# Performance work log

Hardware: AMD Instinct MI355X
Metric: run time of the kernel (lower is better)

The kernel has to match this reference:

```python
import jax, jax.numpy as jnp
import numpy as np

# Tokenizer hyperparams (match init_kwargs)
NUM_VARS = 8
EMBED = 64
WIN = 16
STEP = 4
SWIDTH = 1.0  # sample_width
PWIDTH = 1.0  # patch_width
BATCH = 32
SAMPLES = 4096


def setup_inputs() -> dict:
    key = jax.random.key(0)
    k1, k2, k3, k4, k5 = jax.random.split(key, 5)
    return {
        "x": jax.random.normal(k1, (BATCH, NUM_VARS, SAMPLES), dtype=jnp.float32),
        "W1": jax.random.normal(k2, (NUM_VARS, EMBED), dtype=jnp.float32),   # sample-level LSH hyperplanes
        "b1": jax.random.normal(k3, (EMBED,), dtype=jnp.float32),
        "W2": jax.random.normal(k4, (WIN * EMBED, EMBED), dtype=jnp.float32),  # patch-level LSH hyperplanes
        "b2": jax.random.normal(k5, (EMBED,), dtype=jnp.float32),
    }


def reference(x, W1, b1, W2, b2):
    B, V, S = x.shape
    # encode(): per-timestep sample-level LSH hash, fully vectorized over S.
    # torch loop does sample_level(x[:,:,ix]) for each ix -> one batched einsum here.
    # e: [B, EMBED, S]
    e = jnp.floor((jnp.einsum('bvs,vd->bds', x, W1) + b1[None, :, None]) / SWIDTH)

    # quantize(): sliding windows over the time axis.
    starts = jnp.arange(0, S - WIN, STEP)                 # [T] window start positions
    idx = starts[:, None] + jnp.arange(WIN)[None, :]
    wins = e[:, :, idx]
    T = starts.shape[0]
    flat = wins.transpose(0, 2, 1, 3).reshape(B, T, EMBED * WIN)
    # patch-level LSH hash per window
    tokens = jnp.floor((jnp.einsum('btf,fe->bte', flat, W2) + b2) / PWIDTH)  # [B, T, EMBED]
    return tokens
```

## Files before the change

### kernel.cpp

```cpp
#include <hip/hip_runtime.h>
#include <cstdint>
#include <cstddef>

#define B_ 32
#define V_ 8
#define S_ 4096
#define E_ 64
#define T_ 1020
#define TT 32
#define SLP 200

typedef __bf16 bf16_t;
typedef bf16_t bf16x8 __attribute__((ext_vector_type(8)));
typedef float f32x4 __attribute__((ext_vector_type(4)));
typedef unsigned long long u64;
typedef u64 u64x2 __attribute__((ext_vector_type(2)));

__global__ __launch_bounds__(256) void prep_kernel(const float* __restrict__ W2,
                                                   bf16_t* __restrict__ w2sw) {
  const int q = blockIdx.x * 256 + threadIdx.x;
  const int l = q & 63, nt = (q >> 6) & 3, kk = q >> 8;
  const int fb = kk * 32 + (l >> 4) * 8;
  const int n = nt * 16 + (l & 15);
  bf16x8 v;
#pragma unroll
  for (int j = 0; j < 8; ++j) v[j] = (bf16_t)W2[(fb + j) * E_ + n];
  *reinterpret_cast<bf16x8*>(w2sw + (size_t)q * 8) = v;
}

__global__ __launch_bounds__(256, 4) void fused_kernel(const float* __restrict__ x,
                                                       const float* __restrict__ W1,
                                                       const float* __restrict__ b1,
                                                       const bf16_t* __restrict__ w2sw,
                                                       const float* __restrict__ b2,
                                                       float* __restrict__ out) {
  __shared__ bf16_t et[E_ * SLP];
  const int tid = threadIdx.x;
  const int b = blockIdx.y;
  const int t0 = blockIdx.x * TT;
  const int lane = tid & 63;
  const int wvu = __builtin_amdgcn_readfirstlane(tid >> 6);
  const int l15 = lane & 15;
  const int g = lane >> 4;
  const int s0 = 4 * t0;

  int sc[3];
#pragma unroll
  for (int k = 0; k < 3; ++k) {
    int s = s0 + lane + 64 * k;
    sc[k] = (s > S_ - 1) ? (S_ - 1) : s;
  }
  float xv[V_][3];
#pragma unroll
  for (int v = 0; v < V_; ++v) {
    const float* xb = x + ((size_t)(b * V_ + v) << 12);
#pragma unroll
    for (int k = 0; k < 3; ++k) xv[v][k] = xb[sc[k]];
  }
  const bf16_t* bptr = w2sw + (((size_t)wvu * 64 + lane) << 3);
  bf16x8 bpre[16];
#pragma unroll
  for (int kk = 0; kk < 16; ++kk) {
    bpre[kk] = *reinterpret_cast<const bf16x8*>(bptr + ((size_t)kk << 11));
    u64x2 t = __builtin_bit_cast(u64x2, bpre[kk]);
    asm volatile("" : "+v"(t[0]), "+v"(t[1]));
    bpre[kk] = __builtin_bit_cast(bf16x8, t);
  }

  const int dbase = wvu * 16;
  const float* w1w = W1 + dbase;
  const float* b1w = b1 + dbase;
#pragma unroll
  for (int dd = 0; dd < 16; ++dd) {
    const float bb = b1w[dd];
    float a0 = bb, a1 = bb, a2 = bb;
#pragma unroll
    for (int v = 0; v < V_; ++v) {
      const float w = w1w[v * E_ + dd];
      a0 += xv[v][0] * w;
      a1 += xv[v][1] * w;
      a2 += xv[v][2] * w;
    }
    const int row = (dbase + dd) * SLP;
    et[row + lane]      = (bf16_t)floorf(a0);
    et[row + lane + 64] = (bf16_t)floorf(a1);
    if (lane < 12) et[row + lane + 128] = (bf16_t)floorf(a2);
  }
  __syncthreads();

  const char* etb = reinterpret_cast<const char*>(et);
  const uint32_t aoff = 400u * (g >> 1) + 8u * l15 + 16u * (g & 1);
  const float bv = b2[wvu * 16 + l15];
  f32x4 acc0 = {bv, bv, bv, bv};
  f32x4 acc1 = {bv, bv, bv, bv};
#pragma unroll
  for (int kk = 0; kk < 16; ++kk) {
    const char* pa = etb + aoff + 800 * kk;
    union { u64 q[2]; bf16x8 v; } A0, A1;
    A0.q[0] = *reinterpret_cast<const u64*>(pa);
    A0.q[1] = *reinterpret_cast<const u64*>(pa + 8);
    A1.q[0] = *reinterpret_cast<const u64*>(pa + 128);
    A1.q[1] = *reinterpret_cast<const u64*>(pa + 136);
    acc0 = __builtin_amdgcn_mfma_f32_16x16x32_bf16(A0.v, bpre[kk], acc0, 0, 0, 0);
    acc1 = __builtin_amdgcn_mfma_f32_16x16x32_bf16(A1.v, bpre[kk], acc1, 0, 0, 0);
  }
#pragma unroll 8
  for (int kk = 16; kk < 32; ++kk) {
    const char* pa = etb + aoff + 800 * kk;
    union { u64 q[2]; bf16x8 v; } A0, A1;
    A0.q[0] = *reinterpret_cast<const u64*>(pa);
    A0.q[1] = *reinterpret_cast<const u64*>(pa + 8);
    A1.q[0] = *reinterpret_cast<const u64*>(pa + 128);
    A1.q[1] = *reinterpret_cast<const u64*>(pa + 136);
    const bf16x8 Bf = *reinterpret_cast<const bf16x8*>(bptr + ((size_t)kk << 11));
    acc0 = __builtin_amdgcn_mfma_f32_16x16x32_bf16(A0.v, Bf, acc0, 0, 0, 0);
    acc1 = __builtin_amdgcn_mfma_f32_16x16x32_bf16(A1.v, Bf, acc1, 0, 0, 0);
  }
#pragma unroll
  for (int r = 0; r < 4; ++r) {
    const int t1 = t0 + g * 4 + r;
    if (t1 < T_)
      __builtin_nontemporal_store(floorf(acc0[r]),
                                  &out[((size_t)(b * T_ + t1)) * E_ + wvu * 16 + l15]);
    const int t2 = t0 + 16 + g * 4 + r;
    if (t2 < T_)
      __builtin_nontemporal_store(floorf(acc1[r]),
                                  &out[((size_t)(b * T_ + t2)) * E_ + wvu * 16 + l15]);
  }
}

extern "C" void kernel_launch(void* const* d_in, const int* in_sizes, int n_in,
                              void* d_out, int out_size, void* d_ws, size_t ws_size,
                              hipStream_t stream) {
  const float* x  = (const float*)d_in[0];
  const float* W1 = (const float*)d_in[1];
  const float* b1 = (const float*)d_in[2];
  const float* W2 = (const float*)d_in[3];
  const float* b2 = (const float*)d_in[4];
  float* out = (float*)d_out;

  bf16_t* w2sw = (bf16_t*)d_ws;

  hipLaunchKernelGGL(prep_kernel, dim3(32), dim3(256), 0, stream, W2, w2sw);
  hipLaunchKernelGGL(fused_kernel, dim3((T_ + TT - 1) / TT, B_), dim3(256), 0, stream,
                     x, W1, b1, w2sw, b2, out);
}
```

Measured before the change: 23.17 us.

## Vectorize x loads, pack bf16 LDS stores, drop B-fragment register prefetch

Each lane now loads two adjacent x samples as a float2, plus a small tail handled by six lanes, instead of three strided scalar loads. It writes two bf16 values per 32-bit LDS store instead of single 16-bit stores. The 16-entry register prefetch of W2 fragments, which was overlapped with the sample-level stage, is removed; all 32 k-steps now load B from global memory inside the MFMA loop. This cuts register pressure and LDS store count, at the cost of losing the overlap of B loads with the first stage's compute.

```diff
diff --git a/kernel.cpp b/kernel.cpp
--- a/kernel.cpp
+++ b/kernel.cpp
@@ -14,7 +14,6 @@
 typedef bf16_t bf16x8 __attribute__((ext_vector_type(8)));
 typedef float f32x4 __attribute__((ext_vector_type(4)));
 typedef unsigned long long u64;
-typedef u64 u64x2 __attribute__((ext_vector_type(2)));
 
 __global__ __launch_bounds__(256) void prep_kernel(const float* __restrict__ W2,
                                                    bf16_t* __restrict__ w2sw) {
@@ -26,6 +25,13 @@
 #pragma unroll
   for (int j = 0; j < 8; ++j) v[j] = (bf16_t)W2[(fb + j) * E_ + n];
   *reinterpret_cast<bf16x8*>(w2sw + (size_t)q * 8) = v;
+}
+
+__device__ __forceinline__ uint32_t pack2bf(float a, float b) {
+  union { bf16_t h[2]; uint32_t u; } p;
+  p.h[0] = (bf16_t)a;
+  p.h[1] = (bf16_t)b;
+  return p.u;
 }
 
 __global__ __launch_bounds__(256, 4) void fused_kernel(const float* __restrict__ x,
@@ -44,68 +50,51 @@
   const int g = lane >> 4;
   const int s0 = 4 * t0;
 
-  int sc[3];
-#pragma unroll
-  for (int k = 0; k < 3; ++k) {
-    int s = s0 + lane + 64 * k;
-    sc[k] = (s > S_ - 1) ? (S_ - 1) : s;
-  }
-  float xv[V_][3];
+  float2 xm[V_];
+  float xt0[V_], xt1[V_];
+  const bool htail = lane < 6;
+  int sa = s0 + 128 + 2 * lane, sb = sa + 1;
+  if (sa > S_ - 1) sa = S_ - 1;
+  if (sb > S_ - 1) sb = S_ - 1;
 #pragma unroll
   for (int v = 0; v < V_; ++v) {
     const float* xb = x + ((size_t)(b * V_ + v) << 12);
-#pragma unroll
-    for (int k = 0; k < 3; ++k) xv[v][k] = xb[sc[k]];
-  }
-  const bf16_t* bptr = w2sw + (((size_t)wvu * 64 + lane) << 3);
-  bf16x8 bpre[16];
-#pragma unroll
-  for (int kk = 0; kk < 16; ++kk) {
-    bpre[kk] = *reinterpret_cast<const bf16x8*>(bptr + ((size_t)kk << 11));
-    u64x2 t = __builtin_bit_cast(u64x2, bpre[kk]);
-    asm volatile("" : "+v"(t[0]), "+v"(t[1]));
-    bpre[kk] = __builtin_bit_cast(bf16x8, t);
+    xm[v] = *reinterpret_cast<const float2*>(xb + s0 + 2 * lane);
+    xt0[v] = htail ? xb[sa] : 0.0f;
+    xt1[v] = htail ? xb[sb] : 0.0f;
   }
 
+  char* etc = reinterpret_cast<char*>(et);
   const int dbase = wvu * 16;
-  const float* w1w = W1 + dbase;
-  const float* b1w = b1 + dbase;
 #pragma unroll
   for (int dd = 0; dd < 16; ++dd) {
-    const float bb = b1w[dd];
-    float a0 = bb, a1 = bb, a2 = bb;
+    const int d = dbase + dd;
+    const float bb = b1[d];
+    float a0 = bb, a1 = bb, c0 = bb, c1 = bb;
 #pragma unroll
     for (int v = 0; v < V_; ++v) {
-      const float w = w1w[v * E_ + dd];
-      a0 += xv[v][0] * w;
-      a1 += xv[v][1] * w;
-      a2 += xv[v][2] * w;
+      const float w = W1[v * E_ + d];
+      a0 += xm[v].x * w;
+      a1 += xm[v].y * w;
+      c0 += xt0[v] * w;
+      c1 += xt1[v] * w;
     }
-    const int row = (dbase + dd) * SLP;
-    et[row + lane]      = (bf16_t)floorf(a0);
-    et[row + lane + 64] = (bf16_t)floorf(a1);
-    if (lane < 12) et[row + lane + 128] = (bf16_t)floorf(a2);
+    *reinterpret_cast<uint32_t*>(etc + d * 400 + 4 * lane) =
+        pack2bf(floorf(a0), floorf(a1));
+    if (htail)
+      *reinterpret_cast<uint32_t*>(etc + d * 400 + 256 + 4 * lane) =
+          pack2bf(floorf(c0), floorf(c1));
   }
   __syncthreads();
 
   const char* etb = reinterpret_cast<const char*>(et);
   const uint32_t aoff = 400u * (g >> 1) + 8u * l15 + 16u * (g & 1);
+  const bf16_t* bptr = w2sw + (((size_t)wvu * 64 + lane) << 3);
   const float bv = b2[wvu * 16 + l15];
   f32x4 acc0 = {bv, bv, bv, bv};
   f32x4 acc1 = {bv, bv, bv, bv};
-#pragma unroll
-  for (int kk = 0; kk < 16; ++kk) {
-    const char* pa = etb + aoff + 800 * kk;
-    union { u64 q[2]; bf16x8 v; } A0, A1;
-    A0.q[0] = *reinterpret_cast<const u64*>(pa);
-    A0.q[1] = *reinterpret_cast<const u64*>(pa + 8);
-    A1.q[0] = *reinterpret_cast<const u64*>(pa + 128);
-    A1.q[1] = *reinterpret_cast<const u64*>(pa + 136);
-    acc0 = __builtin_amdgcn_mfma_f32_16x16x32_bf16(A0.v, bpre[kk], acc0, 0, 0, 0);
-    acc1 = __builtin_amdgcn_mfma_f32_16x16x32_bf16(A1.v, bpre[kk], acc1, 0, 0, 0);
-  }
 #pragma unroll 8
-  for (int kk = 16; kk < 32; ++kk) {
+  for (int kk = 0; kk < 32; ++kk) {
     const char* pa = etb + aoff + 800 * kk;
     union { u64 q[2]; bf16x8 v; } A0, A1;
     A0.q[0] = *reinterpret_cast<const u64*>(pa);
```

Result: no change. 22.93 us (-1.1%).
